# Optimization experiments

Measured on AMD Instinct MI355X. Metric: run time of the kernel, lower is better.

The kernel has to match this reference:

```python
import jax, jax.numpy as jnp
import numpy as np

DEPTH = 6


def _interp_linear(x, out_len):
    # x: [B, C, Lin] -> [B, C, out_len], PyTorch mode='linear', align_corners=False
    lin = x.shape[-1]
    scale = lin / out_len
    coords = (jnp.arange(out_len, dtype=x.dtype) + 0.5) * scale - 0.5
    coords = jnp.clip(coords, 0.0, lin - 1)
    lo = jnp.floor(coords).astype(jnp.int32)
    hi = jnp.minimum(lo + 1, lin - 1)
    w = (coords - lo.astype(x.dtype))
    return x[..., lo] * (1.0 - w) + x[..., hi] * w


def _scale_features(x, conv_w, conv_b):
    # x: [B, C, L]; conv_w: [DEPTH, C, C, 3]; conv_b: [DEPTH, C]
    B, C, L = x.shape
    out = x
    for idx in range(DEPTH):
        k = 2 ** (idx + 1)
        pooled = out.reshape(B, C, L // k, k).mean(-1)  # avg_pool1d(kernel=k, stride=k)
        conv = jax.lax.conv_general_dilated(
            pooled, conv_w[idx], window_strides=(1,), padding=((1, 1),),
            dimension_numbers=("NCH", "OIH", "NCH"))
        conv = jax.nn.relu(conv + conv_b[idx][None, :, None])
        out = out + _interp_linear(conv, L)
    return out


def setup_inputs() -> dict:
    key = jax.random.key(0)
    ks = jax.random.split(key, 8)
    N, C = 8192, 512
    s = 1.0 / np.sqrt(C)
    return {
        "features": jax.random.normal(ks[0], (N, C), jnp.float32),
        "Wq": jax.random.normal(ks[1], (C, C), jnp.float32) * s,
        "Wk": jax.random.normal(ks[2], (C, C), jnp.float32) * s,
        "Wv": jax.random.normal(ks[3], (C, C), jnp.float32) * s,
        "Wo": jax.random.normal(ks[4], (C, C), jnp.float32) * s,
        "conv_w": jax.random.normal(ks[5], (DEPTH, C, C, 3), jnp.float32) * (1.0 / np.sqrt(3 * C)),
        "conv_b": jnp.zeros((DEPTH, C), jnp.float32),
        "num_subgraphs": 32,
        "subgraph_len": 256,
    }


def reference(features, Wq, Wk, Wv, Wo, conv_w, conv_b, num_subgraphs, subgraph_len):
    B, L = num_subgraphs, subgraph_len
    N, C = features.shape
    H = 8
    D = C // H
    x = features.reshape(B, L, C)

    # --- per-subgraph multi-head attention (pre_norm path, bn = identity) ---
    q = (x @ Wq).reshape(B, L, H, D)
    k = (x @ Wk).reshape(B, L, H, D)
    v = (x @ Wv).reshape(B, L, H, D)
    scores = jnp.einsum("blhd,bmhd->bhlm", q, k) / jnp.sqrt(jnp.array(D, x.dtype))
    attn = jax.nn.softmax(scores, axis=-1)
    ctx = jnp.einsum("bhlm,bmhd->blhd", attn, v).reshape(B, L, C)
    out = x + ctx @ Wo  # residual (dropout = identity at eval)

    # --- batched ScaleFeatures over subgraphs (ts.scatter.batched equivalent) ---
    local = _scale_features(out.transpose(0, 2, 1), conv_w, conv_b).transpose(0, 2, 1)
    out = out + local
    return out.reshape(N, C)
```

## Files before the change

kernel.cpp:

```cpp
#include <hip/hip_runtime.h>
#include <hip/hip_bf16.h>

typedef __bf16 bf16;
typedef __attribute__((ext_vector_type(8))) __bf16 bf16x8;
typedef __attribute__((ext_vector_type(4))) float f32x4;

#define GLDS16(gp, lp) __builtin_amdgcn_global_load_lds( \
    (const __attribute__((address_space(1))) void*)(gp),  \
    (__attribute__((address_space(3))) void*)(lp), 16, 0, 0)

template<int EPI>
__global__ __launch_bounds__(256)
void gemm_bt(const bf16* __restrict__ A, int lda, long sAb, long sAh,
             const bf16* __restrict__ Bt, int ldb, long sBb, long sBh,
             void* __restrict__ Cp, int ldc, long sCb, long sCh,
             int M, int N, int KC, int tilesN,
             const float* __restrict__ extra, float scale,
             float* __restrict__ C2)
{
    __shared__ __align__(16) bf16 Al[2][128 * 32];
    __shared__ __align__(16) bf16 Bl[2][128 * 32];

    const int t    = threadIdx.x;
    const int lane = t & 63;
    const int w    = t >> 6;
    const int wr   = w >> 1, wc = w & 1;
    const int bid  = blockIdx.x;
    const int batch = blockIdx.y;
    const int tm = bid / tilesN, tn = bid % tilesN;
    const int row0 = tm * 128, col0 = tn * 128;
    const int bb = batch >> 3, bh = batch & 7;
    const int koff = blockIdx.z * KC;

    const bf16* Ab = A  + (long)bb * sAb + (long)bh * sAh;
    const bf16* Bb = Bt + (long)bb * sBb + (long)bh * sBh;

    const int ar0 = t >> 2;
    const int ar1 = (t + 256) >> 2;
    const int ac  = (t & 3) * 8;

    const int arow0 = row0 + ar0, arow1 = row0 + ar1;
    int brow0 = col0 + ar0; if (brow0 > N - 1) brow0 = N - 1;
    int brow1 = col0 + ar1; if (brow1 > N - 1) brow1 = N - 1;

    const long aoff0 = (long)arow0 * lda + koff + ac;
    const long aoff1 = (long)arow1 * lda + koff + ac;
    const long boff0 = (long)brow0 * ldb + koff + ac;
    const long boff1 = (long)brow1 * ldb + koff + ac;

    f32x4 acc[4][4];
#pragma unroll
    for (int i = 0; i < 4; i++)
#pragma unroll
        for (int j = 0; j < 4; j++) acc[i][j] = (f32x4){0.f, 0.f, 0.f, 0.f};

    const int fr = lane & 15, hi = lane >> 4;
    const int nt = KC >> 5;
    int cur = 0;

    GLDS16(Ab + aoff0, &Al[0][w * 512]);
    GLDS16(Ab + aoff1, &Al[0][2048 + w * 512]);
    GLDS16(Bb + boff0, &Bl[0][w * 512]);
    GLDS16(Bb + boff1, &Bl[0][2048 + w * 512]);
    __syncthreads();

    for (int tt = 0; tt < nt; ++tt) {
        if (tt + 1 < nt) {
            const int k1 = (tt + 1) * 32;
            GLDS16(Ab + aoff0 + k1, &Al[cur ^ 1][w * 512]);
            GLDS16(Ab + aoff1 + k1, &Al[cur ^ 1][2048 + w * 512]);
            GLDS16(Bb + boff0 + k1, &Bl[cur ^ 1][w * 512]);
            GLDS16(Bb + boff1 + k1, &Bl[cur ^ 1][2048 + w * 512]);
        }
        bf16x8 af[4], bfr[4];
#pragma unroll
        for (int rt = 0; rt < 4; rt++)
            af[rt] = *(const bf16x8*)&Al[cur][(wr * 64 + rt * 16 + fr) * 32 + hi * 8];
#pragma unroll
        for (int ct = 0; ct < 4; ct++)
            bfr[ct] = *(const bf16x8*)&Bl[cur][(wc * 64 + ct * 16 + fr) * 32 + hi * 8];
#pragma unroll
        for (int rt = 0; rt < 4; rt++)
#pragma unroll
            for (int ct = 0; ct < 4; ct++)
                acc[rt][ct] = __builtin_amdgcn_mfma_f32_16x16x32_bf16(
                    af[rt], bfr[ct], acc[rt][ct], 0, 0, 0);
        __syncthreads();
        cur ^= 1;
    }

    const long cbase = (long)bb * sCb + (long)bh * sCh;
#pragma unroll
    for (int rt = 0; rt < 4; rt++) {
#pragma unroll
        for (int j = 0; j < 4; j++) {
            const int row = row0 + wr * 64 + rt * 16 + hi * 4 + j;
#pragma unroll
            for (int ct = 0; ct < 4; ct++) {
                const int col = col0 + wc * 64 + ct * 16 + fr;
                if (col < N) {
                    const float v = acc[rt][ct][j];
                    const long idx = cbase + (long)row * ldc + col;
                    if constexpr (EPI == 0) {
                        ((bf16*)Cp)[idx] = (bf16)v;
                    } else if constexpr (EPI == 1) {
                        ((float*)Cp)[idx] = v * scale;
                    } else if constexpr (EPI == 2) {
                        const float r = extra[idx] + v;
                        ((float*)Cp)[idx] = r;
                        C2[idx] = r;
                    } else {
                        atomicAdd(((float*)Cp) + idx, v);
                    }
                }
            }
        }
    }
}

__global__ void cvt_f32_bf16(const float* __restrict__ in, bf16* __restrict__ out, int n4)
{
    const int i = blockIdx.x * 256 + threadIdx.x;
    if (i < n4) {
        const float4 v = *(const float4*)&in[(long)i * 4];
        union { bf16 h[4]; ushort4 u; } o;
        o.h[0] = (bf16)v.x; o.h[1] = (bf16)v.y; o.h[2] = (bf16)v.z; o.h[3] = (bf16)v.w;
        *(ushort4*)&out[(long)i * 4] = o.u;
    }
}

__global__ __launch_bounds__(256)
void wtrans(const float* __restrict__ Wq, const float* __restrict__ Wk,
            const float* __restrict__ Wv, const float* __restrict__ Wo,
            bf16* __restrict__ wqkv_t, bf16* __restrict__ wo_t)
{
    __shared__ __align__(16) float T[64][68];
    const int z = blockIdx.z;
    const float* src = (z == 0) ? Wq : (z == 1) ? Wk : (z == 2) ? Wv : Wo;
    bf16* dst = (z < 3) ? (wqkv_t + (long)z * 262144) : wo_t;
    const int r0 = blockIdx.x * 64, c0 = blockIdx.y * 64;
    const int t  = threadIdx.x;
    const int rl = t >> 2;
    const int cq = (t & 3) * 16;
#pragma unroll
    for (int i = 0; i < 4; i++) {
        const float4 v = *(const float4*)&src[(long)(r0 + rl) * 512 + c0 + cq + i * 4];
        T[cq + i * 4 + 0][rl] = v.x;
        T[cq + i * 4 + 1][rl] = v.y;
        T[cq + i * 4 + 2][rl] = v.z;
        T[cq + i * 4 + 3][rl] = v.w;
    }
    __syncthreads();
#pragma unroll
    for (int i = 0; i < 4; i++) {
        const float4 v = *(const float4*)&T[rl][cq + i * 4];
        union { bf16 h[4]; ushort4 u; } o;
        o.h[0] = (bf16)v.x; o.h[1] = (bf16)v.y; o.h[2] = (bf16)v.z; o.h[3] = (bf16)v.w;
        *(ushort4*)&dst[(long)(c0 + rl) * 512 + r0 + cq + i * 4] = o.u;
    }
}

__global__ __launch_bounds__(256)
void vtrans(const bf16* __restrict__ qkv, bf16* __restrict__ vt)
{
    __shared__ __align__(16) bf16 T[64][72];
    const int t  = threadIdx.x;
    const int l0 = blockIdx.x * 64, j0 = blockIdx.y * 64, b = blockIdx.z;
    const int r  = t >> 3;
    const int c8 = (t & 7) * 8;
#pragma unroll
    for (int p = 0; p < 2; p++) {
        const int rr = r + p * 32;
        bf16 v[8];
        *(uint4*)v = *(const uint4*)&qkv[(long)(b * 256 + l0 + rr) * 1536 + 1024 + j0 + c8];
#pragma unroll
        for (int i = 0; i < 8; i++) T[c8 + i][rr] = v[i];
    }
    __syncthreads();
#pragma unroll
    for (int p = 0; p < 2; p++) {
        const int rr = r + p * 32;
        const uint4 val = *(const uint4*)&T[rr][c8];
        *(uint4*)&vt[(long)(b * 512 + j0 + rr) * 256 + l0 + c8] = val;
    }
}

__global__ __launch_bounds__(256)
void softmax_rows(const float* __restrict__ S, bf16* __restrict__ P)
{
    const int row  = blockIdx.x * 4 + (threadIdx.x >> 6);
    const int lane = threadIdx.x & 63;
    const float4 v = *(const float4*)&S[(long)row * 256 + lane * 4];
    float m = fmaxf(fmaxf(v.x, v.y), fmaxf(v.z, v.w));
#pragma unroll
    for (int off = 1; off < 64; off <<= 1) m = fmaxf(m, __shfl_xor(m, off));
    const float e0 = __expf(v.x - m), e1 = __expf(v.y - m);
    const float e2 = __expf(v.z - m), e3 = __expf(v.w - m);
    float s = e0 + e1 + e2 + e3;
#pragma unroll
    for (int off = 1; off < 64; off <<= 1) s += __shfl_xor(s, off);
    const float inv = 1.0f / s;
    union { bf16 h[4]; ushort4 u; } o;
    o.h[0] = (bf16)(e0 * inv); o.h[1] = (bf16)(e1 * inv);
    o.h[2] = (bf16)(e2 * inv); o.h[3] = (bf16)(e3 * inv);
    *(ushort4*)&P[(long)row * 256 + lane * 4] = o.u;
}

__device__ inline void ic_scatter(bf16* __restrict__ icb, int lp, int Ld, float pooled)
{
    const bf16 pb = (bf16)pooled;
    icb[(long)lp * 1536 + 1] = pb;
    if (lp + 1 < Ld) icb[(long)(lp + 1) * 1536] = pb;
    if (lp > 0)      icb[(long)(lp - 1) * 1536 + 2] = pb;
    if (lp == 0)      icb[0] = (bf16)0.f;
    if (lp == Ld - 1) icb[(long)(Ld - 1) * 1536 + 2] = (bf16)0.f;
}

__global__ void cascade_first(const float* __restrict__ sf,
                              bf16* __restrict__ ic,
                              float* __restrict__ convz)
{
    const int idx = blockIdx.x * 256 + threadIdx.x;
    const int c  = idx & 511;
    const int lp = (idx >> 9) & 127;
    const int b  = idx >> 16;
    const float* p = sf + (long)(b * 256 + lp * 2) * 512 + c;
    const float pooled = (p[0] + p[512]) * 0.5f;
    convz[idx] = 0.f;
    ic_scatter(ic + (long)b * 128 * 1536 + (long)c * 3, lp, 128, pooled);
}

__global__ void cascade_mid(const float* __restrict__ conv,
                            const float* __restrict__ bias_p,
                            float* __restrict__ sf,
                            bf16* __restrict__ ic,
                            float* __restrict__ convz,
                            int ldshift, int k, float invk, float scale)
{
    const int idx = blockIdx.x * 256 + threadIdx.x;
    const int Ld = 1 << ldshift;
    const int c  = idx & 511;
    const int lp = (idx >> 9) & (Ld - 1);
    const int b  = idx >> (9 + ldshift);
    const int Lprev = Ld << 1;
    const float bias = bias_p[c];
    float* sfp = sf + ((long)b * 256 + (long)lp * k) * 512 + c;
    const float* cvb = conv + (long)b * Lprev * 512 + c;
    float s = 0.f;
    for (int i = 0; i < k; i++) {
        const int j = lp * k + i;
        float coords = (j + 0.5f) * scale - 0.5f;
        coords = fminf(fmaxf(coords, 0.f), (float)(Lprev - 1));
        const int lo = (int)coords;
        const int hi2 = min(lo + 1, Lprev - 1);
        const float w = coords - (float)lo;
        const float vlo = fmaxf(cvb[(long)lo * 512] + bias, 0.f);
        const float vhi = fmaxf(cvb[(long)hi2 * 512] + bias, 0.f);
        const float v = sfp[(long)i * 512] + vlo * (1.f - w) + vhi * w;
        sfp[(long)i * 512] = v;
        s += v;
    }
    convz[idx] = 0.f;
    ic_scatter(ic + (long)b * Ld * 1536 + (long)c * 3, lp, Ld, s * invk);
}

__global__ void upsample_final(const float* __restrict__ conv,
                               const float* __restrict__ bias_p,
                               const float* __restrict__ sf,
                               float* __restrict__ outp)
{
    const int idx = blockIdx.x * 256 + threadIdx.x;
    const int c = idx & 511;
    const int j = (idx >> 9) & 255;
    const int b = idx >> 17;
    const float bias = bias_p[c];
    float coords = (j + 0.5f) * (4.f / 256.f) - 0.5f;
    coords = fminf(fmaxf(coords, 0.f), 3.f);
    const int lo = (int)coords;
    const int hi2 = min(lo + 1, 3);
    const float w = coords - (float)lo;
    const long rb = (long)b * 4 * 512 + c;
    const float vlo = fmaxf(conv[rb + (long)lo * 512] + bias, 0.f);
    const float vhi = fmaxf(conv[rb + (long)hi2 * 512] + bias, 0.f);
    outp[idx] = outp[idx] + sf[idx] + vlo * (1.f - w) + vhi * w;
}

static const long OFF_XB    = 0;
static const long OFF_WQKV  = 8388608;
static const long OFF_WO    = 9961472;
static const long OFF_WCONV = 10485760;
static const long OFF_QKV   = 19922944;
static const long OFF_VT    = 45088768;
static const long OFF_S     = 53477376;
static const long OFF_CTX   = 53477376;
static const long OFF_IC    = 61865984;
static const long OFF_CONVA = 74448896;
static const long OFF_CONVB = 82837504;
static const long OFF_P     = 120586240;
static const long OFF_SF    = 154140672;

extern "C" void kernel_launch(void* const* d_in, const int* in_sizes, int n_in,
                              void* d_out, int out_size, void* d_ws, size_t ws_size,
                              hipStream_t stream)
{
    const float* features = (const float*)d_in[0];
    const float* Wq = (const float*)d_in[1];
    const float* Wk = (const float*)d_in[2];
    const float* Wv = (const float*)d_in[3];
    const float* Wo = (const float*)d_in[4];
    const float* conv_w = (const float*)d_in[5];
    const float* conv_b = (const float*)d_in[6];
    float* out = (float*)d_out;

    char* ws = (char*)d_ws;
    bf16* xb     = (bf16*)(ws + OFF_XB);
    bf16* wqkv_t = (bf16*)(ws + OFF_WQKV);
    bf16* wo_t   = (bf16*)(ws + OFF_WO);
    bf16* wconv  = (bf16*)(ws + OFF_WCONV);
    bf16* qkv    = (bf16*)(ws + OFF_QKV);
    bf16* vt     = (bf16*)(ws + OFF_VT);
    float* Sbuf  = (float*)(ws + OFF_S);
    bf16* ctx    = (bf16*)(ws + OFF_CTX);
    bf16* ic     = (bf16*)(ws + OFF_IC);
    float* convA = (float*)(ws + OFF_CONVA);
    float* convB = (float*)(ws + OFF_CONVB);
    bf16* P      = (bf16*)(ws + OFF_P);
    float* sf    = (float*)(ws + OFF_SF);
    float* convbuf[2] = {convA, convB};

    cvt_f32_bf16<<<4096, 256, 0, stream>>>(features, xb, 1048576);
    cvt_f32_bf16<<<4608, 256, 0, stream>>>(conv_w, wconv, 1179648);
    wtrans<<<dim3(8, 8, 4), 256, 0, stream>>>(Wq, Wk, Wv, Wo, wqkv_t, wo_t);

    gemm_bt<0><<<dim3(768, 1, 1), 256, 0, stream>>>(
        xb, 512, 0, 0, wqkv_t, 512, 0, 0, qkv, 1536, 0, 0,
        8192, 1536, 512, 12, nullptr, 1.f, nullptr);

    vtrans<<<dim3(4, 8, 32), 256, 0, stream>>>(qkv, vt);

    gemm_bt<1><<<dim3(4, 256, 1), 256, 0, stream>>>(
        qkv, 1536, 393216, 64,
        qkv + 512, 1536, 393216, 64,
        Sbuf, 256, 524288, 65536,
        256, 256, 64, 2, nullptr, 0.125f, nullptr);

    softmax_rows<<<16384, 256, 0, stream>>>(Sbuf, P);

    gemm_bt<0><<<dim3(2, 256, 1), 256, 0, stream>>>(
        P, 256, 524288, 65536,
        vt, 256, 131072, 16384,
        ctx, 512, 131072, 64,
        256, 64, 256, 1, nullptr, 1.f, nullptr);

    gemm_bt<2><<<dim3(256, 1, 1), 256, 0, stream>>>(
        ctx, 512, 0, 0, wo_t, 512, 0, 0, out, 512, 0, 0,
        8192, 512, 512, 4, features, 1.f, sf);

    static const int SPLITS[6] = {2, 4, 8, 12, 12, 12};

    cascade_first<<<8192, 256, 0, stream>>>(sf, ic, convbuf[0]);
    gemm_bt<3><<<dim3(128, 1, SPLITS[0]), 256, 0, stream>>>(
        ic, 1536, 0, 0, wconv, 1536, 0, 0, convbuf[0], 512, 0, 0,
        4096, 512, 1536 / SPLITS[0], 4, nullptr, 1.f, nullptr);

    for (int d = 1; d < 6; d++) {
        const int ldshift = 7 - d;
        const int Ld = 1 << ldshift;
        const int k  = 2 << d;
        cascade_mid<<<64 * Ld, 256, 0, stream>>>(
            convbuf[(d - 1) & 1], conv_b + (d - 1) * 512, sf, ic, convbuf[d & 1],
            ldshift, k, 1.0f / (float)k, (float)(2 * Ld) / 256.f);
        gemm_bt<3><<<dim3((Ld / 4) * 4, 1, SPLITS[d]), 256, 0, stream>>>(
            ic, 1536, 0, 0,
            wconv + (long)d * 786432, 1536, 0, 0,
            convbuf[d & 1], 512, 0, 0,
            32 * Ld, 512, 1536 / SPLITS[d], 4, nullptr, 1.f, nullptr);
    }

    upsample_final<<<16384, 256, 0, stream>>>(
        convbuf[1], conv_b + 5 * 512, sf, out);
}
```

Before: 401.8 us.

## Fuse softmax into QK^T GEMM, split-K output projection, 512-thread GEMM tiles

The generic GEMM now runs 512 threads in an 8-wave 2x4 layout and takes a templated column tile width. The QK^T GEMM covers a full 256-wide row and applies softmax in its epilogue through an LDS cross-wave reduction, so the fp32 score buffer and the separate softmax kernel are gone. The Wo projection now writes two split-K fp32 partials, and cascade_first sums them with the residual to write both out and sf. The conv GEMMs use larger split-K counts, which adds more atomic traffic and more register pressure per block.

```diff
diff --git a/kernel.cpp b/kernel.cpp
--- a/kernel.cpp
+++ b/kernel.cpp
@@ -9,109 +9,188 @@
     (const __attribute__((address_space(1))) void*)(gp),  \
     (__attribute__((address_space(3))) void*)(lp), 16, 0, 0)
 
-template<int EPI>
-__global__ __launch_bounds__(256)
+template<int EPI, int BN>
+__global__ __launch_bounds__(512)
 void gemm_bt(const bf16* __restrict__ A, int lda, long sAb, long sAh,
              const bf16* __restrict__ Bt, int ldb, long sBb, long sBh,
-             void* __restrict__ Cp, int ldc, long sCb, long sCh,
-             int M, int N, int KC, int tilesN,
-             const float* __restrict__ extra, float scale,
-             float* __restrict__ C2)
-{
+             void* __restrict__ Cp, int ldc, long sCb, long sCh, long zC,
+             int KC, int tilesN, float scale)
+{
+    constexpr int CT = BN / 64;
+    constexpr int CW = 16 * CT;
+
     __shared__ __align__(16) bf16 Al[2][128 * 32];
-    __shared__ __align__(16) bf16 Bl[2][128 * 32];
+    __shared__ __align__(16) bf16 Bl[2][BN * 32];
+    __shared__ float red[1024];
 
     const int t    = threadIdx.x;
     const int lane = t & 63;
     const int w    = t >> 6;
-    const int wr   = w >> 1, wc = w & 1;
-    const int bid  = blockIdx.x;
-    const int batch = blockIdx.y;
-    const int tm = bid / tilesN, tn = bid % tilesN;
-    const int row0 = tm * 128, col0 = tn * 128;
-    const int bb = batch >> 3, bh = batch & 7;
+    const int wr   = w >> 2, wc = w & 3;
+    const int tm = blockIdx.x / tilesN, tn = blockIdx.x % tilesN;
+    const int row0 = tm * 128, col0 = tn * BN;
+    const int bb = blockIdx.y >> 3, bh = blockIdx.y & 7;
     const int koff = blockIdx.z * KC;
 
     const bf16* Ab = A  + (long)bb * sAb + (long)bh * sAh;
     const bf16* Bb = Bt + (long)bb * sBb + (long)bh * sBh;
 
-    const int ar0 = t >> 2;
-    const int ar1 = (t + 256) >> 2;
-    const int ac  = (t & 3) * 8;
-
-    const int arow0 = row0 + ar0, arow1 = row0 + ar1;
-    int brow0 = col0 + ar0; if (brow0 > N - 1) brow0 = N - 1;
-    int brow1 = col0 + ar1; if (brow1 > N - 1) brow1 = N - 1;
-
-    const long aoff0 = (long)arow0 * lda + koff + ac;
-    const long aoff1 = (long)arow1 * lda + koff + ac;
-    const long boff0 = (long)brow0 * ldb + koff + ac;
-    const long boff1 = (long)brow1 * ldb + koff + ac;
-
-    f32x4 acc[4][4];
+    const int sr = t >> 2;
+    const int sc = (t & 3) * 8;
+    const long aoff  = (long)(row0 + sr) * lda + koff + sc;
+    const long boff0 = (long)(col0 + sr) * ldb + koff + sc;
+    const long boff1 = (long)(col0 + 128 + sr) * ldb + koff + sc;
+
+    f32x4 acc[4][CT];
 #pragma unroll
     for (int i = 0; i < 4; i++)
 #pragma unroll
-        for (int j = 0; j < 4; j++) acc[i][j] = (f32x4){0.f, 0.f, 0.f, 0.f};
+        for (int j = 0; j < CT; j++) acc[i][j] = (f32x4){0.f, 0.f, 0.f, 0.f};
 
     const int fr = lane & 15, hi = lane >> 4;
     const int nt = KC >> 5;
     int cur = 0;
 
-    GLDS16(Ab + aoff0, &Al[0][w * 512]);
-    GLDS16(Ab + aoff1, &Al[0][2048 + w * 512]);
-    GLDS16(Bb + boff0, &Bl[0][w * 512]);
-    GLDS16(Bb + boff1, &Bl[0][2048 + w * 512]);
+    auto STAGE = [&](int buf, int kk) {
+        GLDS16(Ab + aoff + kk, &Al[buf][w * 512]);
+        if constexpr (BN >= 128) {
+            GLDS16(Bb + boff0 + kk, &Bl[buf][w * 512]);
+            if constexpr (BN == 256)
+                GLDS16(Bb + boff1 + kk, &Bl[buf][4096 + w * 512]);
+        } else {
+            if (w < 4) GLDS16(Bb + boff0 + kk, &Bl[buf][w * 512]);
+        }
+    };
+
+    STAGE(0, 0);
     __syncthreads();
 
     for (int tt = 0; tt < nt; ++tt) {
-        if (tt + 1 < nt) {
-            const int k1 = (tt + 1) * 32;
-            GLDS16(Ab + aoff0 + k1, &Al[cur ^ 1][w * 512]);
-            GLDS16(Ab + aoff1 + k1, &Al[cur ^ 1][2048 + w * 512]);
-            GLDS16(Bb + boff0 + k1, &Bl[cur ^ 1][w * 512]);
-            GLDS16(Bb + boff1 + k1, &Bl[cur ^ 1][2048 + w * 512]);
-        }
-        bf16x8 af[4], bfr[4];
+        if (tt + 1 < nt) STAGE(cur ^ 1, (tt + 1) * 32);
+        bf16x8 af[4], bfr[CT];
 #pragma unroll
         for (int rt = 0; rt < 4; rt++)
             af[rt] = *(const bf16x8*)&Al[cur][(wr * 64 + rt * 16 + fr) * 32 + hi * 8];
 #pragma unroll
-        for (int ct = 0; ct < 4; ct++)
-            bfr[ct] = *(const bf16x8*)&Bl[cur][(wc * 64 + ct * 16 + fr) * 32 + hi * 8];
-#pragma unroll
-        for (int rt = 0; rt < 4; rt++)
-#pragma unroll
-            for (int ct = 0; ct < 4; ct++)
+        for (int ct = 0; ct < CT; ct++)
+            bfr[ct] = *(const bf16x8*)&Bl[cur][(wc * CW + ct * 16 + fr) * 32 + hi * 8];
+#pragma unroll
+        for (int rt = 0; rt < 4; rt++)
+#pragma unroll
+            for (int ct = 0; ct < CT; ct++)
                 acc[rt][ct] = __builtin_amdgcn_mfma_f32_16x16x32_bf16(
                     af[rt], bfr[ct], acc[rt][ct], 0, 0, 0);
         __syncthreads();
         cur ^= 1;
     }
 
-    const long cbase = (long)bb * sCb + (long)bh * sCh;
+    const long cbase = (long)bb * sCb + (long)bh * sCh + (long)blockIdx.z * zC;
+
+    if constexpr (EPI == 4) {
+#pragma unroll
+        for (int rt = 0; rt < 4; rt++)
+#pragma unroll
+            for (int ct = 0; ct < CT; ct++) acc[rt][ct] *= scale;
+
+        float m[4][4];
+#pragma unroll
+        for (int rt = 0; rt < 4; rt++)
+#pragma unroll
+            for (int j = 0; j < 4; j++) {
+                float mm = acc[rt][0][j];
+#pragma unroll
+                for (int ct = 1; ct < CT; ct++) mm = fmaxf(mm, acc[rt][ct][j]);
+#pragma unroll
+                for (int off = 1; off < 16; off <<= 1)
+                    mm = fmaxf(mm, __shfl_xor(mm, off));
+                m[rt][j] = mm;
+            }
+        if (fr == 0) {
+#pragma unroll
+            for (int rt = 0; rt < 4; rt++)
+#pragma unroll
+                for (int j = 0; j < 4; j++)
+                    red[wc * 128 + wr * 64 + rt * 16 + hi * 4 + j] = m[rt][j];
+        }
+        __syncthreads();
+#pragma unroll
+        for (int rt = 0; rt < 4; rt++)
+#pragma unroll
+            for (int j = 0; j < 4; j++) {
+                const int rl = wr * 64 + rt * 16 + hi * 4 + j;
+                m[rt][j] = fmaxf(fmaxf(red[rl], red[128 + rl]),
+                                 fmaxf(red[256 + rl], red[384 + rl]));
+            }
+        float ss[4][4];
+#pragma unroll
+        for (int rt = 0; rt < 4; rt++)
+#pragma unroll
+            for (int j = 0; j < 4; j++) ss[rt][j] = 0.f;
+#pragma unroll
+        for (int rt = 0; rt < 4; rt++)
+#pragma unroll
+            for (int ct = 0; ct < CT; ct++)
+#pragma unroll
+                for (int j = 0; j < 4; j++) {
+                    const float e = __expf(acc[rt][ct][j] - m[rt][j]);
+                    acc[rt][ct][j] = e;
+                    ss[rt][j] += e;
+                }
+#pragma unroll
+        for (int rt = 0; rt < 4; rt++)
+#pragma unroll
+            for (int j = 0; j < 4; j++) {
+#pragma unroll
+                for (int off = 1; off < 16; off <<= 1)
+                    ss[rt][j] += __shfl_xor(ss[rt][j], off);
+            }
+        if (fr == 0) {
+#pragma unroll
+            for (int rt = 0; rt < 4; rt++)
+#pragma unroll
+                for (int j = 0; j < 4; j++)
+                    red[512 + wc * 128 + wr * 64 + rt * 16 + hi * 4 + j] = ss[rt][j];
+        }
+        __syncthreads();
+#pragma unroll
+        for (int rt = 0; rt < 4; rt++)
+#pragma unroll
+            for (int j = 0; j < 4; j++) {
+                const int rl = wr * 64 + rt * 16 + hi * 4 + j;
+                m[rt][j] = 1.f / (red[512 + rl] + red[640 + rl] +
+                                  red[768 + rl] + red[896 + rl]);
+            }
+        bf16* P = (bf16*)Cp;
+#pragma unroll
+        for (int rt = 0; rt < 4; rt++)
+#pragma unroll
+            for (int j = 0; j < 4; j++) {
+                const int row = row0 + wr * 64 + rt * 16 + hi * 4 + j;
+#pragma unroll
+                for (int ct = 0; ct < CT; ct++) {
+                    const int col = col0 + wc * CW + ct * 16 + fr;
+                    P[cbase + (long)row * ldc + col] = (bf16)(acc[rt][ct][j] * m[rt][j]);
+                }
+            }
+        return;
+    }
+
 #pragma unroll
     for (int rt = 0; rt < 4; rt++) {
 #pragma unroll
         for (int j = 0; j < 4; j++) {
             const int row = row0 + wr * 64 + rt * 16 + hi * 4 + j;
 #pragma unroll
-            for (int ct = 0; ct < 4; ct++) {
-                const int col = col0 + wc * 64 + ct * 16 + fr;
-                if (col < N) {
-                    const float v = acc[rt][ct][j];
-                    const long idx = cbase + (long)row * ldc + col;
-                    if constexpr (EPI == 0) {
-                        ((bf16*)Cp)[idx] = (bf16)v;
-                    } else if constexpr (EPI == 1) {
-                        ((float*)Cp)[idx] = v * scale;
-                    } else if constexpr (EPI == 2) {
-                        const float r = extra[idx] + v;
-                        ((float*)Cp)[idx] = r;
-                        C2[idx] = r;
-                    } else {
-                        atomicAdd(((float*)Cp) + idx, v);
-                    }
+            for (int ct = 0; ct < CT; ct++) {
+                const int col = col0 + wc * CW + ct * 16 + fr;
+                const float v = acc[rt][ct][j];
+                const long idx = cbase + (long)row * ldc + col;
+                if constexpr (EPI == 0) {
+                    ((bf16*)Cp)[idx] = (bf16)v;
+                } else if constexpr (EPI == 1) {
+                    ((float*)Cp)[idx] = v * scale;
+                } else {
+                    atomicAdd(((float*)Cp) + idx, v);
                 }
             }
         }
@@ -185,27 +264,6 @@
     }
 }
 
-__global__ __launch_bounds__(256)
-void softmax_rows(const float* __restrict__ S, bf16* __restrict__ P)
-{
-    const int row  = blockIdx.x * 4 + (threadIdx.x >> 6);
-    const int lane = threadIdx.x & 63;
-    const float4 v = *(const float4*)&S[(long)row * 256 + lane * 4];
-    float m = fmaxf(fmaxf(v.x, v.y), fmaxf(v.z, v.w));
-#pragma unroll
-    for (int off = 1; off < 64; off <<= 1) m = fmaxf(m, __shfl_xor(m, off));
-    const float e0 = __expf(v.x - m), e1 = __expf(v.y - m);
-    const float e2 = __expf(v.z - m), e3 = __expf(v.w - m);
-    float s = e0 + e1 + e2 + e3;
-#pragma unroll
-    for (int off = 1; off < 64; off <<= 1) s += __shfl_xor(s, off);
-    const float inv = 1.0f / s;
-    union { bf16 h[4]; ushort4 u; } o;
-    o.h[0] = (bf16)(e0 * inv); o.h[1] = (bf16)(e1 * inv);
-    o.h[2] = (bf16)(e2 * inv); o.h[3] = (bf16)(e3 * inv);
-    *(ushort4*)&P[(long)row * 256 + lane * 4] = o.u;
-}
-
 __device__ inline void ic_scatter(bf16* __restrict__ icb, int lp, int Ld, float pooled)
 {
     const bf16 pb = (bf16)pooled;
@@ -216,7 +274,11 @@
     if (lp == Ld - 1) icb[(long)(Ld - 1) * 1536 + 2] = (bf16)0.f;
 }
 
-__global__ void cascade_first(const float* __restrict__ sf,
+__global__ void cascade_first(const float* __restrict__ features,
+                              const float* __restrict__ p0,
+                              const float* __restrict__ p1,
+                              float* __restrict__ out,
+                              float* __restrict__ sf,
                               bf16* __restrict__ ic,
                               float* __restrict__ convz)
 {
@@ -224,10 +286,14 @@
     const int c  = idx & 511;
     const int lp = (idx >> 9) & 127;
     const int b  = idx >> 16;
-    const float* p = sf + (long)(b * 256 + lp * 2) * 512 + c;
-    const float pooled = (p[0] + p[512]) * 0.5f;
+    const long e0 = (long)(b * 256 + lp * 2) * 512 + c;
+    const long e1 = e0 + 512;
+    const float a0 = features[e0] + p0[e0] + p1[e0];
+    const float a1 = features[e1] + p0[e1] + p1[e1];
+    out[e0] = a0; out[e1] = a1;
+    sf[e0]  = a0; sf[e1]  = a1;
     convz[idx] = 0.f;
-    ic_scatter(ic + (long)b * 128 * 1536 + (long)c * 3, lp, 128, pooled);
+    ic_scatter(ic + (long)b * 128 * 1536 + (long)c * 3, lp, 128, (a0 + a1) * 0.5f);
 }
 
 __global__ void cascade_mid(const float* __restrict__ conv,
@@ -291,12 +357,12 @@
 static const long OFF_WCONV = 10485760;
 static const long OFF_QKV   = 19922944;
 static const long OFF_VT    = 45088768;
-static const long OFF_S     = 53477376;
-static const long OFF_CTX   = 53477376;
-static const long OFF_IC    = 61865984;
-static const long OFF_CONVA = 74448896;
-static const long OFF_CONVB = 82837504;
-static const long OFF_P     = 120586240;
+static const long OFF_P     = 53477376;
+static const long OFF_CTX   = 87031808;
+static const long OFF_WPART = 95420416;
+static const long OFF_IC    = 128974848;
+static const long OFF_CONVA = 141557760;
+static const long OFF_CONVB = 149946368;
 static const long OFF_SF    = 154140672;
 
 extern "C" void kernel_launch(void* const* d_in, const int* in_sizes, int n_in,
@@ -319,12 +385,12 @@
     bf16* wconv  = (bf16*)(ws + OFF_WCONV);
     bf16* qkv    = (bf16*)(ws + OFF_QKV);
     bf16* vt     = (bf16*)(ws + OFF_VT);
-    float* Sbuf  = (float*)(ws + OFF_S);
+    bf16* P      = (bf16*)(ws + OFF_P);
     bf16* ctx    = (bf16*)(ws + OFF_CTX);
+    float* wpart = (float*)(ws + OFF_WPART);
     bf16* ic     = (bf16*)(ws + OFF_IC);
     float* convA = (float*)(ws + OFF_CONVA);
     float* convB = (float*)(ws + OFF_CONVB);
-    bf16* P      = (bf16*)(ws + OFF_P);
     float* sf    = (float*)(ws + OFF_SF);
     float* convbuf[2] = {convA, convB};
 
@@ -332,36 +398,37 @@
     cvt_f32_bf16<<<4608, 256, 0, stream>>>(conv_w, wconv, 1179648);
     wtrans<<<dim3(8, 8, 4), 256, 0, stream>>>(Wq, Wk, Wv, Wo, wqkv_t, wo_t);
 
-    gemm_bt<0><<<dim3(768, 1, 1), 256, 0, stream>>>(
-        xb, 512, 0, 0, wqkv_t, 512, 0, 0, qkv, 1536, 0, 0,
-        8192, 1536, 512, 12, nullptr, 1.f, nullptr);
+    gemm_bt<0, 128><<<dim3(768, 1, 1), 512, 0, stream>>>(
+        xb, 512, 0, 0, wqkv_t, 512, 0, 0, qkv, 1536, 0, 0, 0,
+        512, 12, 1.f);
 
     vtrans<<<dim3(4, 8, 32), 256, 0, stream>>>(qkv, vt);
 
-    gemm_bt<1><<<dim3(4, 256, 1), 256, 0, stream>>>(
+    gemm_bt<4, 256><<<dim3(2, 256, 1), 512, 0, stream>>>(
         qkv, 1536, 393216, 64,
         qkv + 512, 1536, 393216, 64,
-        Sbuf, 256, 524288, 65536,
-        256, 256, 64, 2, nullptr, 0.125f, nullptr);
-
-    softmax_rows<<<16384, 256, 0, stream>>>(Sbuf, P);
-
-    gemm_bt<0><<<dim3(2, 256, 1), 256, 0, stream>>>(
+        P, 256, 524288, 65536, 0,
+        64, 1, 0.125f);
+
+    gemm_bt<0, 64><<<dim3(2, 256, 1), 512, 0, stream>>>(
         P, 256, 524288, 65536,
         vt, 256, 131072, 16384,
-        ctx, 512, 131072, 64,
-        256, 64, 256, 1, nullptr, 1.f, nullptr);
-
-    gemm_bt<2><<<dim3(256, 1, 1), 256, 0, stream>>>(
-        ctx, 512, 0, 0, wo_t, 512, 0, 0, out, 512, 0, 0,
-        8192, 512, 512, 4, features, 1.f, sf);
-
-    static const int SPLITS[6] = {2, 4, 8, 12, 12, 12};
-
-    cascade_first<<<8192, 256, 0, stream>>>(sf, ic, convbuf[0]);
-    gemm_bt<3><<<dim3(128, 1, SPLITS[0]), 256, 0, stream>>>(
-        ic, 1536, 0, 0, wconv, 1536, 0, 0, convbuf[0], 512, 0, 0,
-        4096, 512, 1536 / SPLITS[0], 4, nullptr, 1.f, nullptr);
+        ctx, 512, 131072, 64, 0,
+        256, 1, 1.f);
+
+    gemm_bt<1, 128><<<dim3(256, 1, 2), 512, 0, stream>>>(
+        ctx, 512, 0, 0, wo_t, 512, 0, 0,
+        wpart, 512, 0, 0, 4194304,
+        256, 4, 1.f);
+
+    static const int SPL[6] = {4, 8, 16, 16, 16, 16};
+
+    cascade_first<<<8192, 256, 0, stream>>>(
+        features, wpart, wpart + 4194304, out, sf, ic, convbuf[0]);
+    gemm_bt<3, 128><<<dim3(128, 1, SPL[0]), 512, 0, stream>>>(
+        ic, 1536, 0, 0, wconv, 1536, 0, 0,
+        convbuf[0], 512, 0, 0, 0,
+        1536 / SPL[0], 4, 1.f);
 
     for (int d = 1; d < 6; d++) {
         const int ldshift = 7 - d;
@@ -370,11 +437,11 @@
         cascade_mid<<<64 * Ld, 256, 0, stream>>>(
             convbuf[(d - 1) & 1], conv_b + (d - 1) * 512, sf, ic, convbuf[d & 1],
             ldshift, k, 1.0f / (float)k, (float)(2 * Ld) / 256.f);
-        gemm_bt<3><<<dim3((Ld / 4) * 4, 1, SPLITS[d]), 256, 0, stream>>>(
+        gemm_bt<3, 128><<<dim3((Ld / 4) * 4, 1, SPL[d]), 512, 0, stream>>>(
             ic, 1536, 0, 0,
             wconv + (long)d * 786432, 1536, 0, 0,
-            convbuf[d & 1], 512, 0, 0,
-            32 * Ld, 512, 1536 / SPLITS[d], 4, nullptr, 1.f, nullptr);
+            convbuf[d & 1], 512, 0, 0, 0,
+            1536 / SPL[d], 4, 1.f);
     }
 
     upsample_final<<<16384, 256, 0, stream>>>(
```

Measured after the change: 405.4 us. No clear change (+0.9%).
